# Performance work log

Measured on AMD Instinct MI355X. Metric: run time of the kernel, lower is better.

The kernel has to match this reference:

```python
import jax, jax.numpy as jnp
import numpy as np

N_U = 50000
N_V = 50000
E = 640000
D = 128  # u_dim == v_dim == hid_dim (required for shape consistency)


def setup_inputs() -> dict:
    key = jax.random.key(0)
    ks = jax.random.split(key, 12)
    scale = 1.0 / np.sqrt(D)
    return {
        "X_u": jax.random.normal(ks[0], (N_U, D), dtype=jnp.float32),
        "X_v": jax.random.normal(ks[1], (N_V, D), dtype=jnp.float32),
        "edge_u": jax.random.randint(ks[2], (E,), 0, N_U, dtype=jnp.int32),
        "edge_v": jax.random.randint(ks[3], (E,), 0, N_V, dtype=jnp.int32),
        "W0": jax.random.uniform(ks[4], (D, D), jnp.float32, -scale, scale),
        "b0": jax.random.uniform(ks[5], (D,), jnp.float32, -scale, scale),
        "W1": jax.random.uniform(ks[6], (D, D), jnp.float32, -scale, scale),
        "b1": jax.random.uniform(ks[7], (D,), jnp.float32, -scale, scale),
        "W2": jax.random.uniform(ks[8], (D, D), jnp.float32, -scale, scale),
        "b2": jax.random.uniform(ks[9], (D,), jnp.float32, -scale, scale),
    }


def reference(X_u, X_v, edge_u, edge_v, W0, b0, W1, b1, W2, b2):
    # bipartite scatter-sum aggregations over the edge list
    def v2u(X):  # X: [N_V, D] -> [N_U, D]
        return jax.ops.segment_sum(X[edge_v], edge_u, num_segments=N_U)

    def u2v(X):  # X: [N_U, D] -> [N_V, D]
        return jax.ops.segment_sum(X[edge_u], edge_v, num_segments=N_V)

    # layer 0 (even): Linear(v_dim->hid) on X_v, then v2u sum
    last_X_u = v2u(X_v @ W0 + b0)
    # layer 1 (odd): Linear(u_dim->hid) on last_X_u, then u2v sum
    last_X_v = u2v(last_X_u @ W1 + b1)
    # layer 2 (even): Linear(v_dim->hid) on last_X_v, then v2u sum
    last_X_u = v2u(last_X_v @ W2 + b2)
    return last_X_u
```

## Files before the change

### kernel.cpp

```cpp
#include <hip/hip_runtime.h>

#define D 128
#define NROW 50000
#define NEDGE 640000
#define CAP 64

#define RBLK 160
#define EPB  4000
#define NBKT 196
#define CELL 64

typedef __attribute__((ext_vector_type(8))) short short8;
typedef __attribute__((ext_vector_type(4))) float f32x4;

__device__ __forceinline__ unsigned short f2bf(float f) {
    unsigned u = __float_as_uint(f);
    unsigned r = (u + 0x7fff + ((u >> 16) & 1)) >> 16;
    return (unsigned short)r;
}
__device__ __forceinline__ void acc2(float& e, float& o, unsigned g) {
    e += __uint_as_float(g << 16);
    o += __uint_as_float(g & 0xffff0000u);
}

__global__ __launch_bounds__(256) void route_cvt_gemm1(const int* __restrict__ eu,
                                                       const int* __restrict__ ev,
                                                       unsigned int* __restrict__ recbuf_u,
                                                       int* __restrict__ counts_u,
                                                       unsigned int* __restrict__ recbuf_v,
                                                       int* __restrict__ counts_v,
                                                       const float4* __restrict__ Xv4,
                                                       ushort4* __restrict__ Xb4,
                                                       const float* __restrict__ W0,
                                                       const float* __restrict__ b0,
                                                       const float* __restrict__ b1,
                                                       const float* __restrict__ W1,
                                                       float* __restrict__ T) {
    const int blk = blockIdx.x, tid = threadIdx.x;
    if (blk < 65) {
        __shared__ float R[2][128];
        int sub = tid >> 7, j = tid & 127;
        int i = blk * 2 + sub;
        bool valid = (i < 130);
        const float* row = nullptr;
        if (valid && i < 128) row = W0 + i * D;
        else if (valid && i == 128) row = b0;
        R[sub][j] = row ? row[j] : 0.f;
        __syncthreads();
        if (!valid) return;
        if (i == 129) { T[129 * D + j] = b1[j]; return; }
        float acc = 0.f;
#pragma unroll 8
        for (int k = 0; k < 128; k++) acc += R[sub][k] * W1[k * D + j];
        T[i * D + j] = acc;
    } else if (blk < 225) {
        __shared__ int cnt_s[NBKT];
        __shared__ unsigned int rec_s[NBKT * CELL];
        const int rblk = blk - 65;
        const int base = rblk * EPB;
        for (int dir = 0; dir < 2; dir++) {
            const int* __restrict__ kk = dir ? ev : eu;
            const int* __restrict__ pp = dir ? eu : ev;
            unsigned int* __restrict__ recbuf = dir ? recbuf_v : recbuf_u;
            int* __restrict__ counts = dir ? counts_v : counts_u;
            if (tid < NBKT) cnt_s[tid] = 0;
            __syncthreads();
            for (int e0 = tid; e0 < EPB; e0 += 256) {
                int e = base + e0;
                int key = kk[e], pay = pp[e];
                int k = key >> 8;
                int p = atomicAdd(&cnt_s[k], 1);
                if (p < CELL) rec_s[k * CELL + p] = ((unsigned)key << 16) | (unsigned)pay;
            }
            __syncthreads();
            if (tid < NBKT) {
                int c = cnt_s[tid];
                counts[rblk * NBKT + tid] = (c < CELL) ? c : CELL;
            }
            const int wave = tid >> 6, lane = tid & 63;
            for (int k = wave; k < NBKT; k += 4) {
                int c = cnt_s[k]; c = (c < CELL) ? c : CELL;
                if (lane < c)
                    recbuf[(size_t)(k * RBLK + rblk) * CELL + lane] = rec_s[k * CELL + lane];
            }
            __syncthreads();
        }
    } else {
        int i = (blk - 225) * 256 + tid;
        float4 v = Xv4[i];
        ushort4 o;
        o.x = f2bf(v.x); o.y = f2bf(v.y); o.z = f2bf(v.z); o.w = f2bf(v.w);
        Xb4[i] = o;
    }
}

__global__ __launch_bounds__(256) void ellbuild_sg2(const unsigned int* __restrict__ recbuf_u,
                                                    const int* __restrict__ counts_u,
                                                    const unsigned int* __restrict__ recbuf_v,
                                                    const int* __restrict__ counts_v,
                                                    unsigned short* __restrict__ ell_u,
                                                    int* __restrict__ cnt_u,
                                                    unsigned short* __restrict__ ell_v,
                                                    int* __restrict__ cnt_v,
                                                    const float* __restrict__ T,
                                                    const float* __restrict__ W2,
                                                    float* __restrict__ P,
                                                    unsigned short* __restrict__ PbT) {
    const int blk = blockIdx.x, tid = threadIdx.x;
    if (blk < 2 * NBKT) {
        const int dir = (blk >= NBKT) ? 1 : 0;
        const int k = dir ? blk - NBKT : blk;
        const unsigned int* __restrict__ recbuf = dir ? recbuf_v : recbuf_u;
        const int* __restrict__ counts = dir ? counts_v : counts_u;
        unsigned short* __restrict__ ell = dir ? ell_v : ell_u;
        int* __restrict__ cnt = dir ? cnt_v : cnt_u;

        __shared__ __align__(16) unsigned short ell_s[256 * CAP];
        __shared__ int cnt_s[256];
        __shared__ int seg_c[RBLK];
        cnt_s[tid] = 0;
        if (tid < RBLK) seg_c[tid] = counts[tid * NBKT + k];
        __syncthreads();

        const int wave = tid >> 6, lane = tid & 63;
        const unsigned int* rb = recbuf + (size_t)k * RBLK * CELL;
        int b = wave;
        int c0 = seg_c[b];
        unsigned int r0 = 0;
        if (lane < c0) r0 = rb[b * CELL + lane];
        while (b < RBLK) {
            int bn = b + 4;
            int c1 = 0; unsigned int r1 = 0;
            if (bn < RBLK) { c1 = seg_c[bn]; if (lane < c1) r1 = rb[bn * CELL + lane]; }
            if (lane < c0) {
                int lr = (r0 >> 16) & 255;
                int p = atomicAdd(&cnt_s[lr], 1);
                if (p < CAP) ell_s[lr * CAP + p] = (unsigned short)(r0 & 0xffff);
            }
            b = bn; c0 = c1; r0 = r1;
        }
        __syncthreads();
        const int row0 = k << 8;
        const int nrows = (row0 + 256 <= NROW) ? 256 : (NROW - row0);
        const uint4* src = (const uint4*)ell_s;
        uint4* dst = (uint4*)(ell + (size_t)row0 * CAP);
        for (int i = tid; i < nrows * 8; i += 256) dst[i] = src[i];
        if (tid < nrows) cnt[row0 + tid] = cnt_s[tid];
    } else {
        __shared__ float R[2][128];
        int idx = blk - 2 * NBKT;
        int sub = tid >> 7, j = tid & 127;
        int i = idx * 2 + sub;
        bool valid = (i < 130);
        R[sub][j] = valid ? T[i * D + j] : 0.f;
        __syncthreads();
        if (!valid) return;
        float acc = 0.f;
#pragma unroll 8
        for (int kk = 0; kk < 128; kk++) acc += R[sub][kk] * W2[kk * D + j];
        P[i * D + j] = acc;
        if (i < 128) PbT[j * 128 + i] = f2bf(acc);
    }
}

__device__ __forceinline__ void gather_body(const unsigned short* __restrict__ A,
                                            const int* __restrict__ cnt,
                                            const unsigned short* __restrict__ ell,
                                            unsigned short* __restrict__ OUTb,
                                            int blk) {
    const int r = blk * 16 + (threadIdx.x >> 4);
    const int c = threadIdx.x & 15;
    int n = cnt[r]; n = (n < CAP) ? n : CAP;
    const unsigned short* __restrict__ idx = ell + (size_t)r * CAP;
    const unsigned short* __restrict__ Ac = A + c * 8;
    float a0 = 0.f, a1 = 0.f, a2 = 0.f, a3 = 0.f, a4 = 0.f, a5 = 0.f, a6 = 0.f, a7 = 0.f;
    int i = 0;
    for (; i + 8 <= n; i += 8) {
        uint4 iv = *(const uint4*)(idx + i);
        uint4 q0 = *(const uint4*)(Ac + (size_t)(iv.x & 0xffffu) * D);
        uint4 q1 = *(const uint4*)(Ac + (size_t)(iv.x >> 16) * D);
        uint4 q2 = *(const uint4*)(Ac + (size_t)(iv.y & 0xffffu) * D);
        uint4 q3 = *(const uint4*)(Ac + (size_t)(iv.y >> 16) * D);
        uint4 q4 = *(const uint4*)(Ac + (size_t)(iv.z & 0xffffu) * D);
        uint4 q5 = *(const uint4*)(Ac + (size_t)(iv.z >> 16) * D);
        uint4 q6 = *(const uint4*)(Ac + (size_t)(iv.w & 0xffffu) * D);
        uint4 q7 = *(const uint4*)(Ac + (size_t)(iv.w >> 16) * D);
        acc2(a0, a1, q0.x); acc2(a2, a3, q0.y); acc2(a4, a5, q0.z); acc2(a6, a7, q0.w);
        acc2(a0, a1, q1.x); acc2(a2, a3, q1.y); acc2(a4, a5, q1.z); acc2(a6, a7, q1.w);
        acc2(a0, a1, q2.x); acc2(a2, a3, q2.y); acc2(a4, a5, q2.z); acc2(a6, a7, q2.w);
        acc2(a0, a1, q3.x); acc2(a2, a3, q3.y); acc2(a4, a5, q3.z); acc2(a6, a7, q3.w);
        acc2(a0, a1, q4.x); acc2(a2, a3, q4.y); acc2(a4, a5, q4.z); acc2(a6, a7, q4.w);
        acc2(a0, a1, q5.x); acc2(a2, a3, q5.y); acc2(a4, a5, q5.z); acc2(a6, a7, q5.w);
        acc2(a0, a1, q6.x); acc2(a2, a3, q6.y); acc2(a4, a5, q6.z); acc2(a6, a7, q6.w);
        acc2(a0, a1, q7.x); acc2(a2, a3, q7.y); acc2(a4, a5, q7.z); acc2(a6, a7, q7.w);
    }
    if (i + 4 <= n) {
        uint2 iv = *(const uint2*)(idx + i);
        uint4 q0 = *(const uint4*)(Ac + (size_t)(iv.x & 0xffffu) * D);
        uint4 q1 = *(const uint4*)(Ac + (size_t)(iv.x >> 16) * D);
        uint4 q2 = *(const uint4*)(Ac + (size_t)(iv.y & 0xffffu) * D);
        uint4 q3 = *(const uint4*)(Ac + (size_t)(iv.y >> 16) * D);
        acc2(a0, a1, q0.x); acc2(a2, a3, q0.y); acc2(a4, a5, q0.z); acc2(a6, a7, q0.w);
        acc2(a0, a1, q1.x); acc2(a2, a3, q1.y); acc2(a4, a5, q1.z); acc2(a6, a7, q1.w);
        acc2(a0, a1, q2.x); acc2(a2, a3, q2.y); acc2(a4, a5, q2.z); acc2(a6, a7, q2.w);
        acc2(a0, a1, q3.x); acc2(a2, a3, q3.y); acc2(a4, a5, q3.z); acc2(a6, a7, q3.w);
        i += 4;
    }
    for (; i < n; i++) {
        uint4 q0 = *(const uint4*)(Ac + (size_t)idx[i] * D);
        acc2(a0, a1, q0.x); acc2(a2, a3, q0.y); acc2(a4, a5, q0.z); acc2(a6, a7, q0.w);
    }
    uint4 o;
    o.x = (unsigned)f2bf(a0) | ((unsigned)f2bf(a1) << 16);
    o.y = (unsigned)f2bf(a2) | ((unsigned)f2bf(a3) << 16);
    o.z = (unsigned)f2bf(a4) | ((unsigned)f2bf(a5) << 16);
    o.w = (unsigned)f2bf(a6) | ((unsigned)f2bf(a7) << 16);
    *(uint4*)(OUTb + (size_t)r * D + c * 8) = o;
}

__device__ __forceinline__ void tk_body(const int* __restrict__ cnt_v,
                                        const unsigned short* __restrict__ ell_v,
                                        const int* __restrict__ cnt_u,
                                        int* __restrict__ t, int v) {
    if (v >= NROW) return;
    int n = cnt_v[v]; n = (n < CAP) ? n : CAP;
    const unsigned short* row = ell_v + (size_t)v * CAP;
    int s = 0;
    for (int i = 0; i < n; i += 8) {
        uint4 iv = *(const uint4*)(row + i);
        unsigned sx[8] = {iv.x & 0xffffu, iv.x >> 16, iv.y & 0xffffu, iv.y >> 16,
                          iv.z & 0xffffu, iv.z >> 16, iv.w & 0xffffu, iv.w >> 16};
#pragma unroll
        for (int j = 0; j < 8; j++) if (i + j < n) s += cnt_u[sx[j]];
    }
    t[v] = s;
}

__device__ __forceinline__ void g23_body(const int* __restrict__ cnt_u,
                                         const unsigned short* __restrict__ ell_u,
                                         const int* __restrict__ cnt_v,
                                         const int* __restrict__ t,
                                         int* __restrict__ g2, int* __restrict__ g3, int u) {
    if (u >= NROW) return;
    int n = cnt_u[u]; n = (n < CAP) ? n : CAP;
    const unsigned short* row = ell_u + (size_t)u * CAP;
    int a = 0, b = 0;
    for (int i = 0; i < n; i += 8) {
        uint4 iv = *(const uint4*)(row + i);
        unsigned sx[8] = {iv.x & 0xffffu, iv.x >> 16, iv.y & 0xffffu, iv.y >> 16,
                          iv.z & 0xffffu, iv.z >> 16, iv.w & 0xffffu, iv.w >> 16};
#pragma unroll
        for (int j = 0; j < 8; j++)
            if (i + j < n) { a += t[sx[j]]; b += cnt_v[sx[j]]; }
    }
    g2[u] = a;
    g3[u] = b;
}

__global__ __launch_bounds__(256) void gather1_tk(const unsigned short* __restrict__ A,
                                                  const int* __restrict__ cnt_u,
                                                  const unsigned short* __restrict__ ell_u,
                                                  unsigned short* __restrict__ OUTb,
                                                  const int* __restrict__ cnt_v,
                                                  const unsigned short* __restrict__ ell_v,
                                                  int* __restrict__ t) {
    if (blockIdx.x < 3125) gather_body(A, cnt_u, ell_u, OUTb, blockIdx.x);
    else tk_body(cnt_v, ell_v, cnt_u, t, (blockIdx.x - 3125) * 256 + threadIdx.x);
}

__global__ __launch_bounds__(256) void gather2_g23(const unsigned short* __restrict__ A,
                                                   const int* __restrict__ cnt_v,
                                                   const unsigned short* __restrict__ ell_v,
                                                   unsigned short* __restrict__ OUTb,
                                                   const int* __restrict__ cnt_u,
                                                   const unsigned short* __restrict__ ell_u,
                                                   const int* __restrict__ t,
                                                   int* __restrict__ g2, int* __restrict__ g3) {
    if (blockIdx.x < 3125) gather_body(A, cnt_v, ell_v, OUTb, blockIdx.x);
    else g23_body(cnt_u, ell_u, cnt_v, t, g2, g3, (blockIdx.x - 3125) * 256 + threadIdx.x);
}

__global__ __launch_bounds__(256) void gather_rows(const unsigned short* __restrict__ A,
                                                   const int* __restrict__ cnt,
                                                   const unsigned short* __restrict__ ell,
                                                   unsigned short* __restrict__ OUTb) {
    gather_body(A, cnt, ell, OUTb, blockIdx.x);
}

__global__ __launch_bounds__(256) void gemm_final_mfma(const unsigned short* __restrict__ Z,
                                                       const unsigned short* __restrict__ PbT,
                                                       const float* __restrict__ P,
                                                       const float* __restrict__ b2,
                                                       const int* __restrict__ g2,
                                                       const int* __restrict__ g3,
                                                       const int* __restrict__ du,
                                                       float* __restrict__ OUT) {
    const int wave = threadIdx.x >> 6;
    const int lane = threadIdx.x & 63;
    const int ml = lane & 15;
    const int quad = lane >> 4;
    const int m0 = blockIdx.x * 64 + wave * 16;
    if (m0 >= NROW) return;

    const uint4* zr = (const uint4*)(Z + (size_t)(m0 + ml) * D);

    f32x4 acc[8];
#pragma unroll
    for (int nt = 0; nt < 8; nt++) acc[nt] = (f32x4){0.f, 0.f, 0.f, 0.f};

#pragma unroll
    for (int kc = 0; kc < 4; kc++) {
        short8 a = __builtin_bit_cast(short8, zr[kc * 4 + quad]);
#pragma unroll
        for (int nt = 0; nt < 8; nt++) {
            const uint4* br = (const uint4*)(PbT + (size_t)(nt * 16 + ml) * D);
            short8 b = __builtin_bit_cast(short8, br[kc * 4 + quad]);
            acc[nt] = __builtin_amdgcn_mfma_f32_16x16x32_bf16(a, b, acc[nt], 0, 0, 0);
        }
    }

    float sg2[4], sg3[4], sdu[4];
#pragma unroll
    for (int reg = 0; reg < 4; reg++) {
        int r = m0 + quad * 4 + reg;
        sg2[reg] = (float)g2[r];
        sg3[reg] = (float)g3[r];
        sdu[reg] = (float)du[r];
    }
    const float* c0 = P + 128 * D;
    const float* c1 = P + 129 * D;
#pragma unroll
    for (int nt = 0; nt < 8; nt++) {
        int col = nt * 16 + ml;
        float cc0 = c0[col], cc1 = c1[col], cb2 = b2[col];
#pragma unroll
        for (int reg = 0; reg < 4; reg++) {
            int r = m0 + quad * 4 + reg;
            OUT[(size_t)r * D + col] = acc[nt][reg] + sg2[reg] * cc0 + sg3[reg] * cc1 + sdu[reg] * cb2;
        }
    }
}

extern "C" void kernel_launch(void* const* d_in, const int* in_sizes, int n_in,
                              void* d_out, int out_size, void* d_ws, size_t ws_size,
                              hipStream_t stream) {
    const float* X_v = (const float*)d_in[1];
    const int* edge_u = (const int*)d_in[2];
    const int* edge_v = (const int*)d_in[3];
    const float* W0 = (const float*)d_in[4];
    const float* b0 = (const float*)d_in[5];
    const float* W1 = (const float*)d_in[6];
    const float* b1 = (const float*)d_in[7];
    const float* W2 = (const float*)d_in[8];
    const float* b2 = (const float*)d_in[9];

    char* w = (char*)d_ws;
    unsigned short* A = (unsigned short*)w;
    unsigned short* ell_u = (unsigned short*)(w + 12800000);
    unsigned short* ell_v = ell_u + (size_t)NROW * CAP;
    int* cnt_u = (int*)(ell_v + (size_t)NROW * CAP);
    int* cnt_v = cnt_u + NROW;
    int* tbuf  = cnt_v + NROW;
    int* g2    = tbuf + NROW;
    int* g3    = g2 + NROW;
    float* T   = (float*)(g3 + NROW);
    float* P   = T + 130 * D;
    unsigned short* PbT = (unsigned short*)(P + 130 * D);
    unsigned int* recbuf_u = (unsigned int*)(PbT + 128 * 128);
    unsigned int* recbuf_v = recbuf_u + (size_t)NBKT * RBLK * CELL;
    int* counts_u = (int*)(recbuf_v + (size_t)NBKT * RBLK * CELL);
    int* counts_v = counts_u + NBKT * RBLK;

    float* OUT = (float*)d_out;
    unsigned short* B = (unsigned short*)d_out;

    const dim3 blk(256);

    route_cvt_gemm1<<<65 + RBLK + 6250, blk, 0, stream>>>(edge_u, edge_v,
                                                          recbuf_u, counts_u, recbuf_v, counts_v,
                                                          (const float4*)X_v, (ushort4*)B,
                                                          W0, b0, b1, W1, T);
    ellbuild_sg2<<<2 * NBKT + 65, blk, 0, stream>>>(recbuf_u, counts_u, recbuf_v, counts_v,
                                                    ell_u, cnt_u, ell_v, cnt_v,
                                                    T, W2, P, PbT);
    gather1_tk<<<3125 + 196, blk, 0, stream>>>(B, cnt_u, ell_u, A, cnt_v, ell_v, tbuf);
    gather2_g23<<<3125 + 196, blk, 0, stream>>>(A, cnt_v, ell_v, B, cnt_u, ell_u, tbuf, g2, g3);
    gather_rows<<<3125, blk, 0, stream>>>(B, cnt_u, ell_u, A);
    gemm_final_mfma<<<782, blk, 0, stream>>>(A, PbT, P, b2, g2, g3, cnt_u, OUT);
}
```

Before: 252.4 us.

## Fuse final gather into MFMA GEMM via shared-memory staging

The third gather pass and the final bf16 MFMA GEMM are merged into one kernel. Each block gathers its 64 rows into padded LDS and then runs the MFMA tiles from there. This drops one kernel launch and the global write and re-read of the gathered intermediate. Because the final output now occupies d_out, the intermediate buffer moves from d_out into the route buffer region. The fused kernel has only 782 blocks, so the gather phase runs with less parallelism than the previous 3125-block launch.

```diff
diff --git a/kernel.cpp b/kernel.cpp
--- a/kernel.cpp
+++ b/kernel.cpp
@@ -163,16 +163,9 @@
     }
 }
 
-__device__ __forceinline__ void gather_body(const unsigned short* __restrict__ A,
-                                            const int* __restrict__ cnt,
-                                            const unsigned short* __restrict__ ell,
-                                            unsigned short* __restrict__ OUTb,
-                                            int blk) {
-    const int r = blk * 16 + (threadIdx.x >> 4);
-    const int c = threadIdx.x & 15;
-    int n = cnt[r]; n = (n < CAP) ? n : CAP;
-    const unsigned short* __restrict__ idx = ell + (size_t)r * CAP;
-    const unsigned short* __restrict__ Ac = A + c * 8;
+__device__ __forceinline__ uint4 gather_chunk(const unsigned short* __restrict__ Ac,
+                                              const unsigned short* __restrict__ idx,
+                                              int n) {
     float a0 = 0.f, a1 = 0.f, a2 = 0.f, a3 = 0.f, a4 = 0.f, a5 = 0.f, a6 = 0.f, a7 = 0.f;
     int i = 0;
     for (; i + 8 <= n; i += 8) {
@@ -215,6 +208,18 @@
     o.y = (unsigned)f2bf(a2) | ((unsigned)f2bf(a3) << 16);
     o.z = (unsigned)f2bf(a4) | ((unsigned)f2bf(a5) << 16);
     o.w = (unsigned)f2bf(a6) | ((unsigned)f2bf(a7) << 16);
+    return o;
+}
+
+__device__ __forceinline__ void gather_body(const unsigned short* __restrict__ A,
+                                            const int* __restrict__ cnt,
+                                            const unsigned short* __restrict__ ell,
+                                            unsigned short* __restrict__ OUTb,
+                                            int blk) {
+    const int r = blk * 16 + (threadIdx.x >> 4);
+    const int c = threadIdx.x & 15;
+    int n = cnt[r]; n = (n < CAP) ? n : CAP;
+    uint4 o = gather_chunk(A + c * 8, ell + (size_t)r * CAP, n);
     *(uint4*)(OUTb + (size_t)r * D + c * 8) = o;
 }
 
@@ -280,29 +285,44 @@
     else g23_body(cnt_u, ell_u, cnt_v, t, g2, g3, (blockIdx.x - 3125) * 256 + threadIdx.x);
 }
 
-__global__ __launch_bounds__(256) void gather_rows(const unsigned short* __restrict__ A,
-                                                   const int* __restrict__ cnt,
-                                                   const unsigned short* __restrict__ ell,
-                                                   unsigned short* __restrict__ OUTb) {
-    gather_body(A, cnt, ell, OUTb, blockIdx.x);
-}
-
-__global__ __launch_bounds__(256) void gemm_final_mfma(const unsigned short* __restrict__ Z,
-                                                       const unsigned short* __restrict__ PbT,
-                                                       const float* __restrict__ P,
-                                                       const float* __restrict__ b2,
-                                                       const int* __restrict__ g2,
-                                                       const int* __restrict__ g3,
-                                                       const int* __restrict__ du,
-                                                       float* __restrict__ OUT) {
-    const int wave = threadIdx.x >> 6;
-    const int lane = threadIdx.x & 63;
+#define LSTRIDE 136
+
+__global__ __launch_bounds__(256) void gather3_gemm(const unsigned short* __restrict__ B2,
+                                                    const int* __restrict__ cnt_u,
+                                                    const unsigned short* __restrict__ ell_u,
+                                                    const unsigned short* __restrict__ PbT,
+                                                    const float* __restrict__ P,
+                                                    const float* __restrict__ b2,
+                                                    const int* __restrict__ g2,
+                                                    const int* __restrict__ g3,
+                                                    const int* __restrict__ du,
+                                                    float* __restrict__ OUT) {
+    __shared__ __align__(16) unsigned short Asm[64 * LSTRIDE];
+    const int tid = threadIdx.x;
+    const int m0blk = blockIdx.x * 64;
+
+    const int c = tid & 15;
+#pragma unroll 1
+    for (int it = 0; it < 4; it++) {
+        int rl = (tid >> 4) + it * 16;
+        int r = m0blk + rl;
+        uint4 o = {0u, 0u, 0u, 0u};
+        if (r < NROW) {
+            int n = cnt_u[r]; n = (n < CAP) ? n : CAP;
+            o = gather_chunk(B2 + c * 8, ell_u + (size_t)r * CAP, n);
+        }
+        *(uint4*)(Asm + rl * LSTRIDE + c * 8) = o;
+    }
+    __syncthreads();
+
+    const int wave = tid >> 6;
+    const int lane = tid & 63;
     const int ml = lane & 15;
     const int quad = lane >> 4;
-    const int m0 = blockIdx.x * 64 + wave * 16;
+    const int m0 = m0blk + wave * 16;
     if (m0 >= NROW) return;
 
-    const uint4* zr = (const uint4*)(Z + (size_t)(m0 + ml) * D);
+    const uint4* zr = (const uint4*)(Asm + (size_t)(wave * 16 + ml) * LSTRIDE);
 
     f32x4 acc[8];
 #pragma unroll
@@ -372,19 +392,18 @@
     int* counts_v = counts_u + NBKT * RBLK;
 
     float* OUT = (float*)d_out;
-    unsigned short* B = (unsigned short*)d_out;
-
+    unsigned short* B1 = (unsigned short*)d_out;
+    unsigned short* B2 = (unsigned short*)recbuf_u;
     const dim3 blk(256);
 
     route_cvt_gemm1<<<65 + RBLK + 6250, blk, 0, stream>>>(edge_u, edge_v,
                                                           recbuf_u, counts_u, recbuf_v, counts_v,
-                                                          (const float4*)X_v, (ushort4*)B,
+                                                          (const float4*)X_v, (ushort4*)B1,
                                                           W0, b0, b1, W1, T);
     ellbuild_sg2<<<2 * NBKT + 65, blk, 0, stream>>>(recbuf_u, counts_u, recbuf_v, counts_v,
                                                     ell_u, cnt_u, ell_v, cnt_v,
                                                     T, W2, P, PbT);
-    gather1_tk<<<3125 + 196, blk, 0, stream>>>(B, cnt_u, ell_u, A, cnt_v, ell_v, tbuf);
-    gather2_g23<<<3125 + 196, blk, 0, stream>>>(A, cnt_v, ell_v, B, cnt_u, ell_u, tbuf, g2, g3);
-    gather_rows<<<3125, blk, 0, stream>>>(B, cnt_u, ell_u, A);
-    gemm_final_mfma<<<782, blk, 0, stream>>>(A, PbT, P, b2, g2, g3, cnt_u, OUT);
-}
+    gather1_tk<<<3125 + 196, blk, 0, stream>>>(B1, cnt_u, ell_u, A, cnt_v, ell_v, tbuf);
+    gather2_g23<<<3125 + 196, blk, 0, stream>>>(A, cnt_v, ell_v, B2, cnt_u, ell_u, tbuf, g2, g3);
+    gather3_gemm<<<782, blk, 0, stream>>>(B2, cnt_u, ell_u, PbT, P, b2, g2, g3, cnt_u, OUT);
+}
```

New measurement: 261.2 us. 1.04x slower.
